# Kernel tuning notes

Measured on AMD Instinct MI355X. Metric: run time of the kernel, lower is better.

Reference implementation:

```python
import jax, jax.numpy as jnp
import numpy as np

INF = 1000000000.0
TEMP = 0.1      # dsmax_temperature
THR = 0.2       # confidence threshold
BORDER = 2      # border_rm
H0C, W0C = 60, 80
H1C, W1C = 60, 80
SCALE = 8.0     # hw0_i[0]/hw0_c[0] = 480/60


def setup_inputs() -> dict:
    key = jax.random.key(0)
    k0, k1 = jax.random.split(key)
    N, C = 2, 256
    L = H0C * W0C
    S = H1C * W1C
    feat_c0 = jax.random.normal(k0, (N, L, C), jnp.float32)
    feat_c1 = jax.random.normal(k1, (N, S, C), jnp.float32)
    # padded masks: batch 0 full frame, batch 1 has a smaller valid region
    hi = jnp.arange(H0C)[None, :, None]
    wi = jnp.arange(W0C)[None, None, :]
    h0_valid = jnp.array([H0C, 52])[:, None, None]
    w0_valid = jnp.array([W0C, 72])[:, None, None]
    h1_valid = jnp.array([H1C, 56])[:, None, None]
    w1_valid = jnp.array([W1C, 76])[:, None, None]
    mask0 = (hi < h0_valid) & (wi < w0_valid)   # [N, H0C, W0C] bool
    mask1 = (hi < h1_valid) & (wi < w1_valid)   # [N, H1C, W1C] bool
    return {"feat_c0": feat_c0, "feat_c1": feat_c1, "mask0": mask0, "mask1": mask1}


def _border_valid(mask_hw, hc, wc, n):
    # valid = inside [BORDER, dim_valid - BORDER) per batch (separable in h and w)
    m = mask_hw.astype(jnp.int32)
    hs = jnp.max(jnp.sum(m, axis=1), axis=-1)   # [N] effective heights
    ws = jnp.max(jnp.sum(m, axis=-1), axis=-1)  # [N] effective widths
    hi = jnp.arange(hc)[None, :]
    wi = jnp.arange(wc)[None, :]
    vh = (hi >= BORDER) & (hi < (hs[:, None] - BORDER))  # [N, hc]
    vw = (wi >= BORDER) & (wi < (ws[:, None] - BORDER))  # [N, wc]
    return (vh[:, :, None] & vw[:, None, :]).reshape(n, hc * wc)  # [N, hc*wc]


def reference(feat_c0, feat_c1, mask0, mask1):
    N, L, C = feat_c0.shape
    S = feat_c1.shape[1]
    inv_sqrt_c = 1.0 / (C ** 0.5)
    f0 = feat_c0 * inv_sqrt_c
    f1 = feat_c1 * inv_sqrt_c
    sim = jnp.einsum("nlc,nsc->nls", f0, f1) / TEMP  # [N, L, S]
    mc0 = mask0.reshape(N, L)
    mc1 = mask1.reshape(N, S)
    sim = jnp.where(mc0[:, :, None] & mc1[:, None, :], sim, -INF)
    conf = jax.nn.softmax(sim, axis=1) * jax.nn.softmax(sim, axis=2)  # dual-softmax

    # threshold + padded border removal (separable per-batch border masks)
    valid0 = _border_valid(mask0, H0C, W0C, N)  # [N, L]
    valid1 = _border_valid(mask1, H1C, W1C, N)  # [N, S]
    mask = (conf > THR) & valid0[:, :, None] & valid1[:, None, :]

    # mutual nearest neighbor
    conf_max2 = jnp.max(conf, axis=2, keepdims=True)
    conf_max1 = jnp.max(conf, axis=1, keepdims=True)
    mask = mask & (conf == conf_max2) & (conf == conf_max1)

    # dense match extraction (fixed-shape analogue of torch.where gather)
    mask_v = jnp.any(mask, axis=2)                         # [N, L]
    j_ids = jnp.argmax(mask, axis=2).astype(jnp.int32)     # [N, L] (first True)
    mconf = jnp.take_along_axis(conf, j_ids[..., None].astype(jnp.int32), axis=2)[..., 0]
    mconf = mconf * mask_v                                 # zero where unmatched

    i_ids = jnp.arange(L, dtype=jnp.int32)
    pts0 = jnp.stack([i_ids % W0C, i_ids // W0C], axis=-1).astype(conf.dtype) * SCALE  # [L, 2]
    mkpts0 = jnp.broadcast_to(pts0[None], (N, L, 2))
    mkpts1 = jnp.stack([j_ids % W1C, j_ids // W1C], axis=-1).astype(conf.dtype) * SCALE  # [N, L, 2]
    return conf, mask_v, j_ids, mconf, mkpts0, mkpts1
```

## Files before the change

kernel.cpp:

```cpp
#include <hip/hip_runtime.h>

#define LD 4800
#define SD 4800
#define CD 256
#define H0 60
#define W0 80
#define NB 2
#define THRV 0.2f
#define SIMSCALE 0.0390625f
#define INVL (1.0f/4800.0f)

typedef __attribute__((ext_vector_type(8))) short bf16x8;
typedef __attribute__((ext_vector_type(4))) float f32x4;
typedef __attribute__((ext_vector_type(4))) unsigned short u16x4;
typedef __attribute__((ext_vector_type(8))) unsigned short u16x8;
typedef unsigned long long ull;

__device__ __forceinline__ bool mask_is_u8(const void* m) {
  return ((const unsigned char*)m)[1] != 0;
}
__device__ __forceinline__ bool mask_at(const void* m, int idx, bool u8) {
  return u8 ? (((const unsigned char*)m)[idx] != 0)
            : (((const unsigned int*)m)[idx] != 0u);
}
__device__ __forceinline__ unsigned short f2bf(float x) {
  return (unsigned short)((__float_as_uint(x) + 0x8000u) >> 16);
}


__global__ __launch_bounds__(256)
void prep_kernel(const float* __restrict__ f0, const float* __restrict__ f1,
                 const void* __restrict__ m0, const void* __restrict__ m1,
                 unsigned short* __restrict__ fb0, unsigned short* __restrict__ fb1,
                 unsigned* __restrict__ zws, int* __restrict__ dims, int do_conv) {
  const int t = threadIdx.x;
  const int gid = blockIdx.x * 256 + t;
  const int stride = gridDim.x * 256;
  for (int i = gid; i < 48000; i += stride) zws[i] = 0u;
  if (do_conv) {
    for (int g = gid; g < 614400; g += stride) {
      int gg = g; const float* src; unsigned short* dst;
      if (gg < 307200) { src = f0; dst = fb0; } else { gg -= 307200; src = f1; dst = fb1; }
      size_t off = (size_t)gg * 8;
      f32x4 a = *(const f32x4*)(src + off);
      f32x4 b = *(const f32x4*)(src + off + 4);
      u16x8 o = { f2bf(a.x), f2bf(a.y), f2bf(a.z), f2bf(a.w),
                  f2bf(b.x), f2bf(b.y), f2bf(b.z), f2bf(b.w) };
      *(u16x8*)(dst + off) = o;
    }
  }
  if (blockIdx.x < 4) {
    const bool u8 = mask_is_u8(m0);
    __shared__ short cnt[160];
    const int s = blockIdx.x;
    const void* mm = (s < 2) ? m0 : m1;
    if (s == 0 || s == 2) {
      if (t < NB * W0) {
        int n = t / W0, w = t % W0, c = 0;
        for (int h = 0; h < H0; ++h) c += mask_at(mm, n * LD + h * W0 + w, u8) ? 1 : 0;
        cnt[t] = (short)c;
      }
      __syncthreads();
      if (t < NB) {
        int mx = 0;
        for (int w = 0; w < W0; ++w) mx = max(mx, (int)cnt[t * W0 + w]);
        dims[(s == 0 ? 0 : 4) + t] = mx;
      }
    } else {
      if (t < NB * H0) {
        int n = t / H0, h = t % H0, c = 0;
        for (int w = 0; w < W0; ++w) c += mask_at(mm, n * LD + h * W0 + w, u8) ? 1 : 0;
        cnt[t] = (short)c;
      }
      __syncthreads();
      if (t < NB) {
        int mx = 0;
        for (int h = 0; h < H0; ++h) mx = max(mx, (int)cnt[t * H0 + h]);
        dims[(s == 1 ? 2 : 6) + t] = mx;
      }
    }
  }
}

template<int PASS, int GLL>
__global__ __launch_bounds__(256)
void gemm_fused(const unsigned short* __restrict__ fb0,
                const unsigned short* __restrict__ fb1,
                const float* __restrict__ f0, const float* __restrict__ f1,
                const void* __restrict__ m0, const void* __restrict__ m1,
                float* __restrict__ out, float* __restrict__ rowsum,
                float* __restrict__ colsum, unsigned* __restrict__ colmax,
                ull* __restrict__ rowbest) {
  const int n  = blockIdx.z;
  const int br = blockIdx.y * 128;
  const int bs = blockIdx.x * 128;
  const int t = threadIdx.x;
  const int lane = t & 63, wv = t >> 6;
  const int wr = wv >> 1, wc = wv & 1;
  const int q = lane >> 4, c0 = lane & 15;

  __shared__ unsigned short As[128 * 32];
  __shared__ unsigned short Bs[128 * 32];

  f32x4 acc[4][4] = {};

  if constexpr (GLL) {
    const unsigned short* Ab = fb0 + (size_t)n * LD * CD;
    const unsigned short* Bb = fb1 + (size_t)n * SD * CD;
    const int kk = (t & 3) * 8;
    const int r0 = t >> 2;
    const int gr0 = min(br + r0, LD - 1),      gs0 = min(bs + r0, SD - 1);
    const int gr1 = min(br + r0 + 64, LD - 1), gs1 = min(bs + r0 + 64, SD - 1);
    for (int k0 = 0; k0 < CD; k0 += 32) {
      __syncthreads();
      __builtin_amdgcn_global_load_lds(
          (const __attribute__((address_space(1))) void*)(Ab + (size_t)gr0 * CD + k0 + kk),
          (__attribute__((address_space(3))) void*)(As + wv * 512), 16, 0, 0);
      __builtin_amdgcn_global_load_lds(
          (const __attribute__((address_space(1))) void*)(Ab + (size_t)gr1 * CD + k0 + kk),
          (__attribute__((address_space(3))) void*)(As + 2048 + wv * 512), 16, 0, 0);
      __builtin_amdgcn_global_load_lds(
          (const __attribute__((address_space(1))) void*)(Bb + (size_t)gs0 * CD + k0 + kk),
          (__attribute__((address_space(3))) void*)(Bs + wv * 512), 16, 0, 0);
      __builtin_amdgcn_global_load_lds(
          (const __attribute__((address_space(1))) void*)(Bb + (size_t)gs1 * CD + k0 + kk),
          (__attribute__((address_space(3))) void*)(Bs + 2048 + wv * 512), 16, 0, 0);
      __syncthreads();
      bf16x8 af[4], bfr[4];
#pragma unroll
      for (int m = 0; m < 4; ++m) {
        af[m]  = *(const bf16x8*)(As + (wr * 64 + m * 16 + c0) * 32 + q * 8);
        bfr[m] = *(const bf16x8*)(Bs + (wc * 64 + m * 16 + c0) * 32 + q * 8);
      }
#pragma unroll
      for (int m = 0; m < 4; ++m)
#pragma unroll
        for (int nn = 0; nn < 4; ++nn)
          acc[m][nn] = __builtin_amdgcn_mfma_f32_16x16x32_bf16(af[m], bfr[nn], acc[m][nn], 0, 0, 0);
    }
  } else {
    const float* A = f0 + (size_t)n * LD * CD;
    const float* B = f1 + (size_t)n * SD * CD;
    for (int k0 = 0; k0 < CD; k0 += 32) {
      __syncthreads();
#pragma unroll
      for (int i = 0; i < 4; ++i) {
        int e = (i * 256 + t) * 4;
        int row = e >> 5, k = e & 31;
        int gr = min(br + row, LD - 1), gs = min(bs + row, SD - 1);
        f32x4 va = *(const f32x4*)(A + (size_t)gr * CD + k0 + k);
        f32x4 vb = *(const f32x4*)(B + (size_t)gs * CD + k0 + k);
        u16x4 ua = { f2bf(va.x), f2bf(va.y), f2bf(va.z), f2bf(va.w) };
        u16x4 ub = { f2bf(vb.x), f2bf(vb.y), f2bf(vb.z), f2bf(vb.w) };
        *(u16x4*)(As + row * 32 + k) = ua;
        *(u16x4*)(Bs + row * 32 + k) = ub;
      }
      __syncthreads();
      bf16x8 af[4], bfr[4];
#pragma unroll
      for (int m = 0; m < 4; ++m) {
        af[m]  = *(const bf16x8*)(As + (wr * 64 + m * 16 + c0) * 32 + q * 8);
        bfr[m] = *(const bf16x8*)(Bs + (wc * 64 + m * 16 + c0) * 32 + q * 8);
      }
#pragma unroll
      for (int m = 0; m < 4; ++m)
#pragma unroll
        for (int nn = 0; nn < 4; ++nn)
          acc[m][nn] = __builtin_amdgcn_mfma_f32_16x16x32_bf16(af[m], bfr[nn], acc[m][nn], 0, 0, 0);
    }
  }

  const bool u8 = mask_is_u8(m0);
  int grow[16]; bool inrow[16], mrow[16];
#pragma unroll
  for (int m = 0; m < 4; ++m)
#pragma unroll
    for (int i = 0; i < 4; ++i) {
      int idx = m * 4 + i;
      int r = br + wr * 64 + m * 16 + q * 4 + i;
      grow[idx] = r;
      bool inb = r < LD;
      inrow[idx] = inb;
      mrow[idx] = inb && mask_at(m0, n * LD + (inb ? r : 0), u8);
    }
  int gcol[4]; bool incol[4], mcol[4];
#pragma unroll
  for (int nn = 0; nn < 4; ++nn) {
    int c = bs + wc * 64 + nn * 16 + c0;
    gcol[nn] = c;
    bool inb = c < SD;
    incol[nn] = inb;
    mcol[nn] = inb && mask_at(m1, n * SD + (inb ? c : 0), u8);
  }

  if constexpr (PASS == 0) {
    float rpart[16];
#pragma unroll
    for (int i = 0; i < 16; ++i) rpart[i] = 0.f;
    float cpart[4] = {0.f, 0.f, 0.f, 0.f};
#pragma unroll
    for (int m = 0; m < 4; ++m)
#pragma unroll
      for (int nn = 0; nn < 4; ++nn) {
        f32x4 a = acc[m][nn];
#pragma unroll
        for (int i = 0; i < 4; ++i) {
          int idx = m * 4 + i;
          float val = a[i] * SIMSCALE;
          bool v = mrow[idx] && mcol[nn];
          float e = v ? __expf(val) : 0.f;
          rpart[idx] += e;
          cpart[nn] += e;
        }
      }
#pragma unroll
    for (int idx = 0; idx < 16; ++idx) {
      float s = rpart[idx];
      s += __shfl_xor(s, 1); s += __shfl_xor(s, 2);
      s += __shfl_xor(s, 4); s += __shfl_xor(s, 8);
      if (c0 == 0 && inrow[idx]) atomicAdd(&rowsum[n * LD + grow[idx]], s);
    }
#pragma unroll
    for (int nn = 0; nn < 4; ++nn) {
      float s = cpart[nn];
      s += __shfl_xor(s, 16); s += __shfl_xor(s, 32);
      if (q == 0 && incol[nn]) atomicAdd(&colsum[n * SD + gcol[nn]], s);
    }
  } else {
    float rinv[16];
#pragma unroll
    for (int idx = 0; idx < 16; ++idx)
      rinv[idx] = 1.0f / rowsum[n * LD + (inrow[idx] ? grow[idx] : 0)];
    float cinv[4];
#pragma unroll
    for (int nn = 0; nn < 4; ++nn)
      cinv[nn] = 1.0f / colsum[n * SD + (incol[nn] ? gcol[nn] : 0)];

    ull rkey[16];
#pragma unroll
    for (int i = 0; i < 16; ++i) rkey[i] = 0ull;
    float cmax[4] = {0.f, 0.f, 0.f, 0.f};

#pragma unroll
    for (int m = 0; m < 4; ++m)
#pragma unroll
      for (int nn = 0; nn < 4; ++nn) {
        f32x4 a = acc[m][nn];
#pragma unroll
        for (int i = 0; i < 4; ++i) {
          int idx = m * 4 + i;
          float val = a[i] * SIMSCALE;
          bool v = mrow[idx] && mcol[nn];
          float e = v ? __expf(val) : 0.f;
          float Aa = mrow[idx] ? e * rinv[idx] : INVL;
          float Bb = mcol[nn] ? e * cinv[nn]  : INVL;
          float cv = Aa * Bb;
          bool ok = inrow[idx] && incol[nn];
          if (ok) {
            out[((size_t)n * LD + grow[idx]) * SD + gcol[nn]] = cv;
            cmax[nn] = fmaxf(cmax[nn], cv);
            ull key = ((ull)__float_as_uint(cv) << 32) | (unsigned)(~gcol[nn]);
            if (key > rkey[idx]) rkey[idx] = key;
          }
        }
      }
#pragma unroll
    for (int idx = 0; idx < 16; ++idx) {
      ull key = rkey[idx];
#pragma unroll
      for (int d = 1; d < 16; d <<= 1) {
        ull ok2 = __shfl_xor(key, d);
        key = (ok2 > key) ? ok2 : key;
      }
      if (c0 == 0 && inrow[idx]) atomicMax(&rowbest[n * LD + grow[idx]], key);
    }
#pragma unroll
    for (int nn = 0; nn < 4; ++nn) {
      float s = cmax[nn];
      s = fmaxf(s, __shfl_xor(s, 16));
      s = fmaxf(s, __shfl_xor(s, 32));
      if (q == 0 && incol[nn]) atomicMax(&colmax[n * SD + gcol[nn]], __float_as_uint(s));
    }
  }
}

__global__ void final_kernel(const ull* __restrict__ rowbest,
                             const unsigned* __restrict__ colmax,
                             const int* __restrict__ dims,
                             float* __restrict__ out) {
  const int n = blockIdx.y;
  const int l = blockIdx.x * 256 + threadIdx.x;
  if (l >= LD) return;
  ull key = rowbest[(size_t)n * LD + l];
  float rmax = __uint_as_float((unsigned)(key >> 32));
  int j = (int)(~(unsigned)(key & 0xFFFFFFFFull));
  if (j < 0 || j >= SD) j = 0;
  const int hs0 = dims[0 + n], ws0 = dims[2 + n], hs1 = dims[4 + n], ws1 = dims[6 + n];
  const int h = l / W0, w = l % W0;
  const bool v0 = (h >= 2) && (h < hs0 - 2) && (w >= 2) && (w < ws0 - 2);
  const int jh = j / W0, jw = j % W0;
  const bool v1 = (jh >= 2) && (jh < hs1 - 2) && (jw >= 2) && (jw < ws1 - 2);
  const float cmx = __uint_as_float(colmax[(size_t)n * SD + j]);
  const bool mv = (rmax > THRV) && v0 && v1 && (rmax == cmx);
  const int jid = mv ? j : 0;

  const size_t base = (size_t)NB * LD * SD;
  const int NL = NB * LD;
  out[base + (size_t)n * LD + l]                  = mv ? 1.f : 0.f;
  out[base + NL + (size_t)n * LD + l]             = (float)jid;
  out[base + 2 * (size_t)NL + (size_t)n * LD + l] = mv ? rmax : 0.f;
  size_t mk0 = base + 3 * (size_t)NL + ((size_t)n * LD + l) * 2;
  out[mk0 + 0] = (float)(w * 8);
  out[mk0 + 1] = (float)(h * 8);
  size_t mk1 = base + 5 * (size_t)NL + ((size_t)n * LD + l) * 2;
  out[mk1 + 0] = (float)((jid % W0) * 8);
  out[mk1 + 1] = (float)((jid / W0) * 8);
}

extern "C" void kernel_launch(void* const* d_in, const int* in_sizes, int n_in,
                              void* d_out, int out_size, void* d_ws, size_t ws_size,
                              hipStream_t stream) {
  (void)in_sizes; (void)n_in; (void)out_size;
  const float* f0 = (const float*)d_in[0];
  const float* f1 = (const float*)d_in[1];
  const void*  m0 = d_in[2];
  const void*  m1 = d_in[3];
  float* out = (float*)d_out;
  char* ws = (char*)d_ws;

  const size_t FB_BYTES = (size_t)NB * LD * CD * 2;
  const bool gll = ws_size >= 2 * FB_BYTES + 192032;

  unsigned short* fb0 = gll ? (unsigned short*)ws : nullptr;
  unsigned short* fb1 = gll ? (unsigned short*)(ws + FB_BYTES) : nullptr;
  char* sums = gll ? (ws + 2 * FB_BYTES) : ws;

  float* rowsum = (float*)sums;
  float* colsum = (float*)(sums + 38400);
  unsigned* colmax = (unsigned*)(sums + 76800);
  ull* rowbest = (ull*)(sums + 115200);
  int* dims = (int*)(sums + 192000);

  prep_kernel<<<512, 256, 0, stream>>>(f0, f1, m0, m1, fb0, fb1,
                                       (unsigned*)sums, dims, gll ? 1 : 0);
  if (gll) {
    gemm_fused<0, 1><<<dim3(38, 38, 2), 256, 0, stream>>>(
        fb0, fb1, f0, f1, m0, m1, out, rowsum, colsum, colmax, rowbest);
    gemm_fused<1, 1><<<dim3(38, 38, 2), 256, 0, stream>>>(
        fb0, fb1, f0, f1, m0, m1, out, rowsum, colsum, colmax, rowbest);
  } else {
    gemm_fused<0, 0><<<dim3(38, 38, 2), 256, 0, stream>>>(
        fb0, fb1, f0, f1, m0, m1, out, rowsum, colsum, colmax, rowbest);
    gemm_fused<1, 0><<<dim3(38, 38, 2), 256, 0, stream>>>(
        fb0, fb1, f0, f1, m0, m1, out, rowsum, colsum, colmax, rowbest);
  }
  final_kernel<<<dim3(19, 2), 256, 0, stream>>>(rowbest, colmax, dims, out);
}
```

Measured before the change: 419.1 us.

## Store bf16 exp matrix once and stream conf instead of recomputing GEMM

```diff
diff --git a/kernel.cpp b/kernel.cpp
--- a/kernel.cpp
+++ b/kernel.cpp
@@ -25,6 +25,9 @@
 }
 __device__ __forceinline__ unsigned short f2bf(float x) {
   return (unsigned short)((__float_as_uint(x) + 0x8000u) >> 16);
+}
+__device__ __forceinline__ float bf2f(unsigned short u) {
+  return __uint_as_float(((unsigned)u) << 16);
 }
 
 
@@ -77,6 +80,230 @@
         int mx = 0;
         for (int h = 0; h < H0; ++h) mx = max(mx, (int)cnt[t * H0 + h]);
         dims[(s == 1 ? 2 : 6) + t] = mx;
+      }
+    }
+  }
+}
+
+__global__ __launch_bounds__(256)
+void gemm_e(const unsigned short* __restrict__ fb0,
+            const unsigned short* __restrict__ fb1,
+            const void* __restrict__ m0, const void* __restrict__ m1,
+            unsigned short* __restrict__ eb, float* __restrict__ rowsum,
+            float* __restrict__ colsum) {
+  const int n  = blockIdx.z;
+  const int br = blockIdx.y * 128;
+  const int bs = blockIdx.x * 128;
+  const int t = threadIdx.x;
+  const int lane = t & 63, wv = t >> 6;
+  const int wr = wv >> 1, wc = wv & 1;
+  const int q = lane >> 4, c0 = lane & 15;
+
+  __shared__ unsigned short lds[16384];
+  unsigned short* As = lds;
+  unsigned short* Bs = lds + 8192;
+
+  const unsigned short* Ab = fb0 + (size_t)n * LD * CD;
+  const unsigned short* Bb = fb1 + (size_t)n * SD * CD;
+
+  const int rloc = lane >> 3;
+  const int cch  = (lane & 7) ^ rloc;
+
+  f32x4 acc[4][4] = {};
+
+  for (int k0 = 0; k0 < CD; k0 += 64) {
+    __syncthreads();
+#pragma unroll
+    for (int j = 0; j < 4; ++j) {
+      int rl = wv * 32 + j * 8 + rloc;
+      int ra = min(br + rl, LD - 1);
+      int rb = min(bs + rl, SD - 1);
+      __builtin_amdgcn_global_load_lds(
+          (const __attribute__((address_space(1))) void*)(Ab + (size_t)ra * CD + k0 + cch * 8),
+          (__attribute__((address_space(3))) void*)(As + (wv * 32 + j * 8) * 64), 16, 0, 0);
+      __builtin_amdgcn_global_load_lds(
+          (const __attribute__((address_space(1))) void*)(Bb + (size_t)rb * CD + k0 + cch * 8),
+          (__attribute__((address_space(3))) void*)(Bs + (wv * 32 + j * 8) * 64), 16, 0, 0);
+    }
+    __syncthreads();
+#pragma unroll
+    for (int kk2 = 0; kk2 < 2; ++kk2) {
+      bf16x8 af[4], bfr[4];
+#pragma unroll
+      for (int m = 0; m < 4; ++m) {
+        int pa = ((kk2 << 2) + q) ^ (c0 & 7);
+        af[m]  = *(const bf16x8*)(As + (wr * 64 + m * 16 + c0) * 64 + pa * 8);
+        bfr[m] = *(const bf16x8*)(Bs + (wc * 64 + m * 16 + c0) * 64 + pa * 8);
+      }
+#pragma unroll
+      for (int m = 0; m < 4; ++m)
+#pragma unroll
+        for (int nn = 0; nn < 4; ++nn)
+          acc[m][nn] = __builtin_amdgcn_mfma_f32_16x16x32_bf16(af[m], bfr[nn], acc[m][nn], 0, 0, 0);
+    }
+  }
+
+  const bool u8 = mask_is_u8(m0);
+  int grow[16]; bool inrow[16], mrow[16];
+#pragma unroll
+  for (int m = 0; m < 4; ++m)
+#pragma unroll
+    for (int i = 0; i < 4; ++i) {
+      int idx = m * 4 + i;
+      int r = br + wr * 64 + m * 16 + q * 4 + i;
+      grow[idx] = r;
+      bool inb = r < LD;
+      inrow[idx] = inb;
+      mrow[idx] = inb && mask_at(m0, n * LD + (inb ? r : 0), u8);
+    }
+  int gcol[4]; bool incol[4], mcol[4];
+#pragma unroll
+  for (int nn = 0; nn < 4; ++nn) {
+    int c = bs + wc * 64 + nn * 16 + c0;
+    gcol[nn] = c;
+    bool inb = c < SD;
+    incol[nn] = inb;
+    mcol[nn] = inb && mask_at(m1, n * SD + (inb ? c : 0), u8);
+  }
+
+  __syncthreads();
+
+  float rpart[16];
+#pragma unroll
+  for (int i = 0; i < 16; ++i) rpart[i] = 0.f;
+  float cpart[4] = {0.f, 0.f, 0.f, 0.f};
+
+#pragma unroll
+  for (int m = 0; m < 4; ++m)
+#pragma unroll
+    for (int nn = 0; nn < 4; ++nn) {
+      f32x4 a = acc[m][nn];
+#pragma unroll
+      for (int i = 0; i < 4; ++i) {
+        int idx = m * 4 + i;
+        float val = a[i] * SIMSCALE;
+        bool v = mrow[idx] && mcol[nn];
+        float ef = v ? __expf(val) : 0.f;
+        rpart[idx] += ef;
+        cpart[nn] += ef;
+        float es = v ? ef : ((!mrow[idx] && !mcol[nn]) ? 1.f : 0.f);
+        int row = wr * 64 + m * 16 + q * 4 + i;
+        int col = wc * 64 + nn * 16 + c0;
+        int byte = (row * 256 + col * 2) ^ ((row & 12) << 3);
+        *(unsigned short*)((char*)lds + byte) = f2bf(es);
+      }
+    }
+
+#pragma unroll
+  for (int idx = 0; idx < 16; ++idx) {
+    float s = rpart[idx];
+    s += __shfl_xor(s, 1); s += __shfl_xor(s, 2);
+    s += __shfl_xor(s, 4); s += __shfl_xor(s, 8);
+    if (c0 == 0 && inrow[idx]) atomicAdd(&rowsum[n * LD + grow[idx]], s);
+  }
+#pragma unroll
+  for (int nn = 0; nn < 4; ++nn) {
+    float s = cpart[nn];
+    s += __shfl_xor(s, 16); s += __shfl_xor(s, 32);
+    if (q == 0 && incol[nn]) atomicAdd(&colsum[n * SD + gcol[nn]], s);
+  }
+
+  __syncthreads();
+  const size_t ebase = (size_t)n * LD * SD;
+#pragma unroll
+  for (int it = 0; it < 8; ++it) {
+    int row = it * 16 + (t >> 4);
+    int col = (t & 15) * 8;
+    int gr = br + row, gc = bs + col;
+    if (gr < LD && gc < SD) {
+      int byte = (row * 256 + col * 2) ^ ((row & 12) << 3);
+      u16x8 v = *(u16x8*)((char*)lds + byte);
+      *(u16x8*)(eb + ebase + (size_t)gr * SD + gc) = v;
+    }
+  }
+}
+
+__global__ void inv_kernel(const float* __restrict__ rowsum, const float* __restrict__ colsum,
+                           const void* __restrict__ m0, const void* __restrict__ m1,
+                           float* __restrict__ rinv, float* __restrict__ cinv) {
+  int i = blockIdx.x * 256 + threadIdx.x;
+  if (i >= NB * LD) return;
+  const bool u8 = mask_is_u8(m0);
+  rinv[i] = mask_at(m0, i, u8) ? (1.0f / rowsum[i]) : INVL;
+  cinv[i] = mask_at(m1, i, u8) ? (1.0f / colsum[i]) : INVL;
+}
+
+__global__ __launch_bounds__(256)
+void conf_stream(const unsigned short* __restrict__ eb, const float* __restrict__ rinv,
+                 const float* __restrict__ cinv, float* __restrict__ out,
+                 unsigned* __restrict__ colmax, ull* __restrict__ rowbest) {
+  const int t = threadIdx.x, lane = t & 63, wv = t >> 6;
+  const int row0 = blockIdx.x * 8;
+  const int n = row0 / LD;
+  const int r0 = row0 % LD;
+
+  __shared__ float civ[4800];
+  __shared__ ull rb_s[8][4];
+  for (int i = t; i < 4800; i += 256) civ[i] = cinv[n * SD + i];
+  __syncthreads();
+
+  float cm[3][8];
+#pragma unroll
+  for (int k = 0; k < 3; ++k)
+#pragma unroll
+    for (int j = 0; j < 8; ++j) cm[k][j] = 0.f;
+
+  for (int rr = 0; rr < 8; ++rr) {
+    const int r = r0 + rr;
+    const float ri = rinv[n * LD + r];
+    const unsigned short* erow = eb + ((size_t)n * LD + r) * SD;
+    float* crow = out + ((size_t)n * LD + r) * SD;
+    ull tb = 0ull;
+#pragma unroll
+    for (int k = 0; k < 3; ++k) {
+      int ch = t + k * 256;
+      if (ch < 600) {
+        int c = ch * 8;
+        u16x8 ev = *(const u16x8*)(erow + c);
+        f32x4 lo, hi;
+#pragma unroll
+        for (int j = 0; j < 8; ++j) {
+          float e = bf2f(ev[j]);
+          float cf = (e * ri) * (e * civ[c + j]);
+          if (j < 4) lo[j] = cf; else hi[j - 4] = cf;
+          cm[k][j] = fmaxf(cm[k][j], cf);
+          ull key = ((ull)__float_as_uint(cf) << 32) | (unsigned)(~(c + j));
+          tb = (key > tb) ? key : tb;
+        }
+        *(f32x4*)(crow + c) = lo;
+        *(f32x4*)(crow + c + 4) = hi;
+      }
+    }
+#pragma unroll
+    for (int d = 1; d < 64; d <<= 1) {
+      ull o = __shfl_xor(tb, d);
+      tb = (o > tb) ? o : tb;
+    }
+    if (lane == 0) rb_s[rr][wv] = tb;
+  }
+  __syncthreads();
+  if (t < 8) {
+    ull b0 = rb_s[t][0], b1 = rb_s[t][1], b2 = rb_s[t][2], b3 = rb_s[t][3];
+    ull b = b0 > b1 ? b0 : b1;
+    ull c2 = b2 > b3 ? b2 : b3;
+    b = b > c2 ? b : c2;
+    rowbest[(size_t)n * LD + r0 + t] = b;
+  }
+#pragma unroll
+  for (int k = 0; k < 3; ++k) {
+    int ch = t + k * 256;
+    if (ch < 600) {
+      int c = ch * 8;
+#pragma unroll
+      for (int j = 0; j < 8; ++j) {
+        unsigned mine = __float_as_uint(cm[k][j]);
+        unsigned cur = colmax[n * SD + c + j];
+        if (mine > cur) atomicMax(&colmax[n * SD + c + j], mine);
       }
     }
   }
@@ -329,21 +556,32 @@
   char* ws = (char*)d_ws;
 
   const size_t FB_BYTES = (size_t)NB * LD * CD * 2;
-  const bool gll = ws_size >= 2 * FB_BYTES + 192032;
-
-  unsigned short* fb0 = gll ? (unsigned short*)ws : nullptr;
-  unsigned short* fb1 = gll ? (unsigned short*)(ws + FB_BYTES) : nullptr;
-  char* sums = gll ? (ws + 2 * FB_BYTES) : ws;
+  const size_t SUMS_OFF = 2 * FB_BYTES;
+  const size_t E_OFF    = 10099456;
+  const size_t TIER_A   = E_OFF + (size_t)NB * LD * SD * 2;
+  const bool tierA = ws_size >= TIER_A;
+  const bool tierB = !tierA && ws_size >= SUMS_OFF + 270000;
+
+  char* sums = (tierA || tierB) ? (ws + SUMS_OFF) : ws;
+  unsigned short* fb0 = (tierA || tierB) ? (unsigned short*)ws : nullptr;
+  unsigned short* fb1 = (tierA || tierB) ? (unsigned short*)(ws + FB_BYTES) : nullptr;
 
   float* rowsum = (float*)sums;
   float* colsum = (float*)(sums + 38400);
   unsigned* colmax = (unsigned*)(sums + 76800);
   ull* rowbest = (ull*)(sums + 115200);
   int* dims = (int*)(sums + 192000);
+  float* rinv = (float*)(sums + 192064);
+  float* cinv = (float*)(sums + 230464);
+  unsigned short* eb = (unsigned short*)(ws + E_OFF);
 
   prep_kernel<<<512, 256, 0, stream>>>(f0, f1, m0, m1, fb0, fb1,
-                                       (unsigned*)sums, dims, gll ? 1 : 0);
-  if (gll) {
+                                       (unsigned*)sums, dims, (tierA || tierB) ? 1 : 0);
+  if (tierA) {
+    gemm_e<<<dim3(38, 38, 2), 256, 0, stream>>>(fb0, fb1, m0, m1, eb, rowsum, colsum);
+    inv_kernel<<<38, 256, 0, stream>>>(rowsum, colsum, m0, m1, rinv, cinv);
+    conf_stream<<<1200, 256, 0, stream>>>(eb, rinv, cinv, out, colmax, rowbest);
+  } else if (tierB) {
     gemm_fused<0, 1><<<dim3(38, 38, 2), 256, 0, stream>>>(
         fb0, fb1, f0, f1, m0, m1, out, rowsum, colsum, colmax, rowbest);
     gemm_fused<1, 1><<<dim3(38, 38, 2), 256, 0, stream>>>(
```

After: 659.4 us. 57.4% more time.
